# Performance work log

Measured on AMD Instinct MI355X. Metric: run time of the kernel, lower is better.

## Reference

```python
import jax, jax.numpy as jnp
import numpy as np

B, S, D = 8, 2048, 64
H = 128


def setup_inputs() -> dict:
    key = jax.random.key(0)
    k = jax.random.split(key, 5)
    X = jax.random.normal(k[0], (B, S, D), dtype=jnp.float32)
    Wi = jax.random.normal(k[1], (H, D), dtype=jnp.float32)          # init_layer weight, std=1
    bi = jax.random.normal(k[2], (H,), dtype=jnp.float32)            # init_layer bias, std=1
    Wa = jax.random.normal(k[3], (H * H, D + 1), dtype=jnp.float32) / jnp.sqrt(H)  # vf_A, std=1/sqrt(H)
    Wb = jax.random.normal(k[4], (H, D + 1), dtype=jnp.float32)      # vf_B, std=1
    return {"X": X, "Wi": Wi, "bi": bi, "Wa": Wa, "Wb": Wb}


def reference(X, Wi, bi, Wa, Wb):
    b, s, d = X.shape
    dt = 1.0 / (s - 1)
    # inp: time channel (constant dt) concatenated with scaled input -> [b, s, d+1]
    inp = jnp.concatenate([jnp.full((b, s, 1), dt, dtype=X.dtype), X * dt], axis=-1)
    y0 = X[:, 0] @ Wi.T + bi                       # [b, H]
    Bs = jnp.einsum('bsk,hk->bsh', inp[:, 1:], Wb)  # [b, s-1, H]

    def step(y, xs):
        inp_t, b_t = xs                            # [b, d+1], [b, H]
        A = (inp_t @ Wa.T).reshape(b, H, H)        # per-step transition matrix
        y_new = y + jnp.einsum('bij,bj->bi', A, y) + b_t
        return y_new, y_new

    xs = (jnp.swapaxes(inp[:, 1:], 0, 1), jnp.swapaxes(Bs, 0, 1))  # time-major
    _, ys_rest = jax.lax.scan(step, y0, xs)        # [s-1, b, H]
    ys = jnp.concatenate([y0[:, None, :], jnp.swapaxes(ys_rest, 0, 1)], axis=1)
    return ys
```

## Files before the change

### kernel.cpp

```cpp
#include <hip/hip_runtime.h>
#include <hip/hip_fp16.h>


typedef _Float16 h8 __attribute__((ext_vector_type(8)));
typedef float v4f __attribute__((ext_vector_type(4)));
typedef unsigned int uint;

constexpr int B_ = 8, S_ = 2048, D_ = 64, H_ = 128;
constexpr int T_ = S_ - 1;
constexpr int KD = D_ + 1;
constexpr float DTC = 1.0f / 2047.0f;
constexpr int L_ = 8;
constexpr int LSH = 3;
constexpr int NC = 256;

__global__ __launch_bounds__(256) void k_prep0(const float* __restrict__ Wa,
                                               _Float16* __restrict__ Wa16B,
                                               float* __restrict__ Wa0,
                                               const float* __restrict__ X,
                                               _Float16* __restrict__ Xs16) {
  int bx = blockIdx.x;
  if (bx < 4096) {
    int idx = bx * 256 + threadIdx.x;
    int r = idx >> 6, kk = idx & 63;
    int rt = r >> 4, n = r & 15;
    int kb = kk >> 5, q = (kk >> 3) & 3, jj = kk & 7;
    float v = Wa[(size_t)r * KD + 1 + kk];
    Wa16B[((((size_t)rt * 2 + kb) * 4 + q) * 16 + n) * 8 + jj] = (_Float16)v;
    if (kk == 0) Wa0[r] = Wa[(size_t)r * KD];
  } else {
    int idx = (bx - 4096) * 256 + threadIdx.x;
    if (idx < B_ * T_ * 64) {
      int bt = idx >> 6, d = idx & 63;
      int b = bt / T_, s = bt - b * T_;
      Xs16[(size_t)bt * 64 + d] = (_Float16)(X[((size_t)b * S_ + s + 1) * D_ + d] * DTC);
    }
  }
}

__global__ __launch_bounds__(256) void k_prep1(const float* __restrict__ X,
                                               const float* __restrict__ Wb,
                                               float* __restrict__ Bs,
                                               const float* __restrict__ Wi,
                                               const float* __restrict__ bi,
                                               float* __restrict__ out,
                                               float* __restrict__ yb) {
  int tid = threadIdx.x;
  if (blockIdx.x >= 1024) {
    int b = blockIdx.x - 1024;
    __shared__ float xs0[D_];
    if (tid < D_) xs0[tid] = X[(size_t)b * S_ * D_ + tid];
    __syncthreads();
    if (tid < H_) {
      float acc = bi[tid];
      const float* wr = Wi + tid * D_;
#pragma unroll 8
      for (int d = 0; d < D_; d++) acc += xs0[d] * wr[d];
      out[(size_t)b * S_ * H_ + tid] = acc;
      yb[(size_t)(b * NC + 0) * H_ + tid] = acc;
    }
    return;
  }
  __shared__ float wb_s[H_ * KD];
  __shared__ float xs[16][D_ + 4];
  int bt0 = blockIdx.x * 16;
  for (int i = tid; i < H_ * KD; i += 256) wb_s[i] = Wb[i];
  for (int i = tid; i < 16 * D_; i += 256) {
    int sl = i >> 6, d = i & 63;
    int btg = bt0 + sl;
    float v = 0.f;
    if (btg < B_ * T_) {
      int b = btg / T_, s = btg - b * T_;
      v = X[((size_t)b * S_ + s + 1) * D_ + d] * DTC;
    }
    xs[sl][d] = v;
  }
  __syncthreads();
  int h = tid & 127, sh = tid >> 7;
  const float* wrow = &wb_s[h * KD];
  for (int u = 0; u < 8; u++) {
    int sl = sh * 8 + u;
    int btg = bt0 + sl;
    if (btg >= B_ * T_) break;
    float acc = wrow[0] * DTC;
#pragma unroll 8
    for (int d = 0; d < D_; d++) acc += xs[sl][d] * wrow[1 + d];
    Bs[(size_t)btg * H_ + h] = acc;
  }
}

__global__ __launch_bounds__(256) void k_amat(const _Float16* __restrict__ Xs16,
                                              const _Float16* __restrict__ Wa16B,
                                              const float* __restrict__ Wa0,
                                              _Float16* __restrict__ A_sl,
                                              int c0, int scShift) {
  __shared__ _Float16 sb[32 * 528];
  int tid = threadIdx.x;
  int w = tid >> 6, lane = tid & 63;
  int n = lane & 15, q = lane >> 4;
  int rowbase = blockIdx.x * 32;
  int SCm = ((1 << scShift) << LSH) - 1;

  h8 af[2][2];
#pragma unroll
  for (int mi = 0; mi < 2; mi++) {
    int sidx = rowbase + mi * 16 + n;
    int b = sidx >> (scShift + LSH);
    int rem = sidx & SCm;
    int cc = rem >> LSH, l = rem & (L_ - 1);
    int s = (c0 + cc) * L_ + l;
    if (s >= T_) s = T_ - 1;
    size_t btg = (size_t)b * T_ + s;
#pragma unroll
    for (int kb = 0; kb < 2; kb++)
      af[mi][kb] = *(const h8*)(Xs16 + btg * 64 + kb * 32 + q * 8);
  }

  v4f acc[2][8];
#pragma unroll
  for (int nj = 0; nj < 8; nj++) {
    int ct_g = blockIdx.y * 32 + w * 8 + nj;
    float binit = DTC * Wa0[ct_g * 16 + n];
    h8 bf0 = *(const h8*)(Wa16B + ((((size_t)ct_g * 2 + 0) * 4 + q) * 16 + n) * 8);
    h8 bf1 = *(const h8*)(Wa16B + ((((size_t)ct_g * 2 + 1) * 4 + q) * 16 + n) * 8);
#pragma unroll
    for (int mi = 0; mi < 2; mi++) {
      v4f a;
      a[0] = binit; a[1] = binit; a[2] = binit; a[3] = binit;
      a = __builtin_amdgcn_mfma_f32_16x16x32_f16(af[mi][0], bf0, a, 0, 0, 0);
      a = __builtin_amdgcn_mfma_f32_16x16x32_f16(af[mi][1], bf1, a, 0, 0, 0);
      acc[mi][nj] = a;
    }
  }
#pragma unroll
  for (int mi = 0; mi < 2; mi++)
#pragma unroll
    for (int nj = 0; nj < 8; nj++)
#pragma unroll
      for (int reg = 0; reg < 4; reg++)
        sb[(mi * 16 + q * 4 + reg) * 528 + w * 128 + ((nj * 16 + n) ^ (q * 16))] =
            (_Float16)acc[mi][nj][reg];
  __syncthreads();
#pragma unroll
  for (int it = 0; it < 8; it++) {
    int idx = tid + it * 256;
    int t = idx >> 6, u4 = idx & 63;
    int qt = (t >> 2) & 3;
    uint4 val = *(const uint4*)&sb[t * 528 + ((u4 * 8) ^ (qt * 16))];
    *(uint4*)(A_sl + (size_t)(rowbase + t) * 16384 + blockIdx.y * 512 + u4 * 8) = val;
  }
}

__global__ __launch_bounds__(256) void k_chunkmap(const _Float16* __restrict__ A_sl,
                                                  const float* __restrict__ Bs,
                                                  _Float16* __restrict__ Mr,
                                                  float* __restrict__ vch,
                                                  int c0, int scShift) {
  __shared__ _Float16 Dt[128 * 136];
  __shared__ float v32[128];
  int tid = threadIdx.x;
  int w = tid >> 6, lane = tid & 63;
  int n = lane & 15, q = lane >> 4;
  int chunk = blockIdx.x;
  int SC = 1 << scShift;
  int b = chunk >> scShift;
  int cc = chunk & (SC - 1);
  int c = c0 + cc;
  int sbase = c * L_;
  int nsteps = min(L_, T_ - sbase);
  const _Float16* Abase = A_sl + (size_t)chunk * L_ * 16384;
  size_t btb = (size_t)b * T_ + sbase;

#pragma unroll
  for (int it = 0; it < 8; it++) {
    int idx = tid + it * 256;
    int rowl = idx & 127, c8 = (idx >> 7) * 8;
    uint4 pk = *(const uint4*)(Abase + rowl * 128 + c8);
    const _Float16* hp = (const _Float16*)&pk;
#pragma unroll
    for (int cx = 0; cx < 8; cx++) Dt[(c8 + cx) * 136 + rowl] = hp[cx];
  }
  if (tid < 128) v32[tid] = Bs[btb * 128 + tid];
  h8 idE, idO;
#pragma unroll
  for (int jj = 0; jj < 8; jj++) {
    idE[jj] = (_Float16)((q * 8 + jj == n) ? 1.f : 0.f);
    idO[jj] = (_Float16)((q * 8 + jj == 16 + n) ? 1.f : 0.f);
  }
  __syncthreads();

  v4f acc[2][8];
#pragma unroll
  for (int mi = 0; mi < 2; mi++) {
    int row0 = (2 * w + mi) * 16 + q * 4;
#pragma unroll
    for (int nj = 0; nj < 8; nj++) {
      int col = nj * 16 + n;
      union { uint2 u; _Float16 h[4]; } m2;
      m2.u = *(const uint2*)&Dt[col * 136 + row0];
#pragma unroll
      for (int reg = 0; reg < 4; reg++) acc[mi][nj][reg] = (float)m2.h[reg];
    }
  }

  int r0 = 2 * w * 16 + n, r1 = r0 + 16;
  h8 afA[2][4], afB[2][4];

#define LOADA(dst, l)                                                                \
  {                                                                                  \
    const _Float16* Ag = Abase + (size_t)(l) * 16384;                                \
    _Pragma("unroll")                                                                \
    for (int mi = 0; mi < 2; mi++)                                                   \
      _Pragma("unroll")                                                              \
      for (int kb = 0; kb < 4; kb++)                                                 \
        dst[mi][kb] = *(const h8*)(Ag + ((2 * w + mi) * 16 + n) * 128 + kb * 32 + q * 8); \
  }

#define STEPQ(af, l)                                                                 \
  {                                                                                  \
    _Pragma("unroll")                                                                \
    for (int nj = 0; nj < 8; nj++) {                                                 \
      h8 bfr[4];                                                                     \
      _Pragma("unroll")                                                              \
      for (int kb = 0; kb < 4; kb++)                                                 \
        bfr[kb] = *(const h8*)&Dt[(nj * 16 + n) * 136 + kb * 32 + q * 8];            \
      _Pragma("unroll")                                                              \
      for (int mi = 0; mi < 2; mi++) {                                               \
        _Pragma("unroll")                                                            \
        for (int kb = 0; kb < 4; kb++)                                               \
          acc[mi][nj] = __builtin_amdgcn_mfma_f32_16x16x32_f16(af[mi][kb], bfr[kb], acc[mi][nj], 0, 0, 0); \
        acc[mi][nj] = __builtin_amdgcn_mfma_f32_16x16x32_f16(                        \
            af[mi][nj >> 1], (nj & 1) ? idO : idE, acc[mi][nj], 0, 0, 0);            \
      }                                                                              \
    }                                                                                \
    float dv0 = 0.f, dv1 = 0.f;                                                      \
    _Pragma("unroll")                                                                \
    for (int kb = 0; kb < 4; kb++) {                                                 \
      float4 p0 = *(const float4*)&v32[kb * 32 + q * 8];                             \
      float4 p1 = *(const float4*)&v32[kb * 32 + q * 8 + 4];                         \
      float vk[8] = {p0.x, p0.y, p0.z, p0.w, p1.x, p1.y, p1.z, p1.w};                \
      _Pragma("unroll")                                                              \
      for (int jj = 0; jj < 8; jj++) {                                               \
        dv0 += (float)af[0][kb][jj] * vk[jj];                                        \
        dv1 += (float)af[1][kb][jj] * vk[jj];                                        \
      }                                                                              \
    }                                                                                \
    dv0 += __shfl_xor(dv0, 16); dv0 += __shfl_xor(dv0, 32);                          \
    dv1 += __shfl_xor(dv1, 16); dv1 += __shfl_xor(dv1, 32);                          \
    float vold0 = v32[r0], vold1 = v32[r1];                                          \
    float bs0 = 0.f, bs1 = 0.f;                                                      \
    if (q == 0) {                                                                    \
      bs0 = Bs[(btb + (l)) * 128 + r0];                                              \
      bs1 = Bs[(btb + (l)) * 128 + r1];                                              \
    }                                                                                \
    __syncthreads();                                                                 \
    _Pragma("unroll")                                                                \
    for (int mi = 0; mi < 2; mi++) {                                                 \
      int row0 = (2 * w + mi) * 16 + q * 4;                                          \
      _Pragma("unroll")                                                              \
      for (int nj = 0; nj < 8; nj++) {                                               \
        int col = nj * 16 + n;                                                       \
        union { _Float16 h[4]; uint2 u; } pk;                                        \
        _Pragma("unroll")                                                            \
        for (int reg = 0; reg < 4; reg++) pk.h[reg] = (_Float16)acc[mi][nj][reg];    \
        *(uint2*)&Dt[col * 136 + row0] = pk.u;                                       \
      }                                                                              \
    }                                                                                \
    if (q == 0) {                                                                    \
      v32[r0] = vold0 + dv0 + bs0;                                                   \
      v32[r1] = vold1 + dv1 + bs1;                                                   \
    }                                                                                \
    __syncthreads();                                                                 \
  }

  LOADA(afA, 1);
  for (int l = 1; l < nsteps; l += 2) {
    if (l + 1 < nsteps) LOADA(afB, l + 1);
    STEPQ(afA, l);
    if (l + 2 < nsteps) LOADA(afA, l + 2);
    if (l + 1 < nsteps) STEPQ(afB, l + 1);
  }
#undef LOADA
#undef STEPQ

#pragma unroll
  for (int mi = 0; mi < 2; mi++) {
    int row0 = (2 * w + mi) * 16 + q * 4;
#pragma unroll
    for (int nj = 0; nj < 8; nj++) {
      int col = nj * 16 + n;
#pragma unroll
      for (int reg = 0; reg < 4; reg++)
        Dt[(row0 + reg) * 136 + col] = (_Float16)acc[mi][nj][reg];
    }
  }
  __syncthreads();
  _Float16* og = Mr + (size_t)chunk * 16384;
#pragma unroll
  for (int it = 0; it < 8; it++) {
    int idx = tid + it * 256;
    int rowl = idx >> 4, ch = idx & 15;
    uint4 val = *(const uint4*)&Dt[rowl * 136 + ch * 8];
    *(uint4*)(og + rowl * 128 + ch * 8) = val;
  }
  if (tid < 128) vch[(size_t)chunk * 128 + tid] = v32[tid];
}

__global__ __launch_bounds__(256) void k_comp4(const _Float16* __restrict__ in_map,
                                               const float* __restrict__ in_v,
                                               _Float16* __restrict__ out_map,
                                               float* __restrict__ out_v) {
  __shared__ _Float16 Dt[128 * 136];
  __shared__ float v32[128];
  int tid = threadIdx.x;
  int w = tid >> 6, lane = tid & 63;
  int n = lane & 15, q = lane >> 4;
  size_t nbase = (size_t)blockIdx.x * 4;

  const _Float16* P0 = in_map + nbase * 16384;
#pragma unroll
  for (int it = 0; it < 8; it++) {
    int idx = tid + it * 256;
    int rowl = idx & 127, c8 = (idx >> 7) * 8;
    uint4 pk = *(const uint4*)(P0 + rowl * 128 + c8);
    const _Float16* hp = (const _Float16*)&pk;
#pragma unroll
    for (int cx = 0; cx < 8; cx++) Dt[(c8 + cx) * 136 + rowl] = hp[cx];
  }
  if (tid < 128) v32[tid] = in_v[nbase * 128 + tid];
  h8 idE, idO;
#pragma unroll
  for (int jj = 0; jj < 8; jj++) {
    idE[jj] = (_Float16)((q * 8 + jj == n) ? 1.f : 0.f);
    idO[jj] = (_Float16)((q * 8 + jj == 16 + n) ? 1.f : 0.f);
  }
  __syncthreads();

  v4f acc[2][8];
#pragma unroll
  for (int mi = 0; mi < 2; mi++) {
    int row0 = (2 * w + mi) * 16 + q * 4;
#pragma unroll
    for (int nj = 0; nj < 8; nj++) {
      int col = nj * 16 + n;
      union { uint2 u; _Float16 h[4]; } m2;
      m2.u = *(const uint2*)&Dt[col * 136 + row0];
#pragma unroll
      for (int reg = 0; reg < 4; reg++) acc[mi][nj][reg] = (float)m2.h[reg];
    }
  }

  int r0 = 2 * w * 16 + n, r1 = r0 + 16;
  for (int j = 1; j < 4; j++) {
    const _Float16* Pj = in_map + (nbase + j) * 16384;
    h8 af[2][4];
#pragma unroll
    for (int mi = 0; mi < 2; mi++)
#pragma unroll
      for (int kb = 0; kb < 4; kb++)
        af[mi][kb] = *(const h8*)(Pj + ((2 * w + mi) * 16 + n) * 128 + kb * 32 + q * 8);
#pragma unroll
    for (int nj = 0; nj < 8; nj++) {
      h8 bfr[4];
#pragma unroll
      for (int kb = 0; kb < 4; kb++)
        bfr[kb] = *(const h8*)&Dt[(nj * 16 + n) * 136 + kb * 32 + q * 8];
#pragma unroll
      for (int mi = 0; mi < 2; mi++) {
#pragma unroll
        for (int kb = 0; kb < 4; kb++)
          acc[mi][nj] = __builtin_amdgcn_mfma_f32_16x16x32_f16(af[mi][kb], bfr[kb], acc[mi][nj], 0, 0, 0);
        acc[mi][nj] = __builtin_amdgcn_mfma_f32_16x16x32_f16(
            af[mi][nj >> 1], (nj & 1) ? idO : idE, acc[mi][nj], 0, 0, 0);
      }
    }
    float dv0 = 0.f, dv1 = 0.f;
#pragma unroll
    for (int kb = 0; kb < 4; kb++) {
      float4 p0 = *(const float4*)&v32[kb * 32 + q * 8];
      float4 p1 = *(const float4*)&v32[kb * 32 + q * 8 + 4];
      float vk[8] = {p0.x, p0.y, p0.z, p0.w, p1.x, p1.y, p1.z, p1.w};
#pragma unroll
      for (int jj = 0; jj < 8; jj++) {
        dv0 += (float)af[0][kb][jj] * vk[jj];
        dv1 += (float)af[1][kb][jj] * vk[jj];
      }
    }
    dv0 += __shfl_xor(dv0, 16); dv0 += __shfl_xor(dv0, 32);
    dv1 += __shfl_xor(dv1, 16); dv1 += __shfl_xor(dv1, 32);
    float vold0 = v32[r0], vold1 = v32[r1];
    float vj0 = 0.f, vj1 = 0.f;
    if (q == 0) {
      vj0 = in_v[(nbase + j) * 128 + r0];
      vj1 = in_v[(nbase + j) * 128 + r1];
    }
    __syncthreads();
#pragma unroll
    for (int mi = 0; mi < 2; mi++) {
      int row0 = (2 * w + mi) * 16 + q * 4;
#pragma unroll
      for (int nj = 0; nj < 8; nj++) {
        int col = nj * 16 + n;
        union { _Float16 h[4]; uint2 u; } pk;
#pragma unroll
        for (int reg = 0; reg < 4; reg++) pk.h[reg] = (_Float16)acc[mi][nj][reg];
        *(uint2*)&Dt[col * 136 + row0] = pk.u;
      }
    }
    if (q == 0) {
      v32[r0] = vold0 + dv0 + vj0;
      v32[r1] = vold1 + dv1 + vj1;
    }
    __syncthreads();
  }
#pragma unroll
  for (int mi = 0; mi < 2; mi++) {
    int row0 = (2 * w + mi) * 16 + q * 4;
#pragma unroll
    for (int nj = 0; nj < 8; nj++) {
      int col = nj * 16 + n;
#pragma unroll
      for (int reg = 0; reg < 4; reg++)
        Dt[(row0 + reg) * 136 + col] = (_Float16)acc[mi][nj][reg];
    }
  }
  __syncthreads();
  _Float16* og = out_map + (size_t)blockIdx.x * 16384;
#pragma unroll
  for (int it = 0; it < 8; it++) {
    int idx = tid + it * 256;
    int rowl = idx >> 4, ch = idx & 15;
    uint4 val = *(const uint4*)&Dt[rowl * 136 + ch * 8];
    *(uint4*)(og + rowl * 128 + ch * 8) = val;
  }
  if (tid < 128) out_v[(size_t)blockIdx.x * 128 + tid] = v32[tid];
}

__global__ __launch_bounds__(256) void k_chainsuper(const _Float16* __restrict__ Sr,
                                                    const float* __restrict__ sv,
                                                    float* __restrict__ yb,
                                                    int c0, int scShift) {
  int b = blockIdx.x, tid = threadIdx.x;
  int NS = 1 << (scShift - 2);
  int i = tid >> 1, hh = tid & 1;
  __shared__ float ybuf[128];
  __shared__ float red[128];
  if (tid < 128) ybuf[tid] = yb[(size_t)(b * NC + c0) * 128 + tid];
  __syncthreads();

  uint4 arA[8], arB[8];
  float svA, svB;

#define LOADS(ar, svv, s)                                                            \
  {                                                                                  \
    const uint4* p = (const uint4*)(Sr + (size_t)(b * NS + (s)) * 16384 + i * 128 + hh * 64); \
    _Pragma("unroll")                                                                \
    for (int u = 0; u < 8; u++) ar[u] = p[u];                                        \
    svv = sv[(size_t)(b * NS + (s)) * 128 + i];                                      \
  }

#define STEPS(ar, svv, s)                                                            \
  {                                                                                  \
    float pt = 0.f;                                                                  \
    _Pragma("unroll")                                                                \
    for (int u = 0; u < 8; u++) {                                                    \
      union { uint4 v; _Float16 h[8]; } wv; wv.v = ar[u];                            \
      _Pragma("unroll")                                                              \
      for (int k = 0; k < 8; k++) pt += (float)wv.h[k] * ybuf[hh * 64 + u * 8 + k];  \
    }                                                                                \
    if (hh) red[i] = pt;                                                             \
    __syncthreads();                                                                 \
    if (!hh) {                                                                       \
      float yn = ybuf[i] + pt + red[i] + svv;                                        \
      int cg = c0 + 4 * ((s) + 1);                                                   \
      if (cg < NC) yb[(size_t)(b * NC + cg) * 128 + i] = yn;                         \
      ybuf[i] = yn;                                                                  \
    }                                                                                \
    __syncthreads();                                                                 \
  }

  LOADS(arA, svA, 0);
  int s = 0;
  for (; s + 1 < NS; s += 2) {
    LOADS(arB, svB, s + 1);
    STEPS(arA, svA, s);
    if (s + 2 < NS) LOADS(arA, svA, s + 2);
    STEPS(arB, svB, s + 1);
  }
  if (s < NS) STEPS(arA, svA, s);
#undef LOADS
#undef STEPS
}

__global__ __launch_bounds__(256) void k_emit(const _Float16* __restrict__ A_sl,
                                              const float* __restrict__ Bs,
                                              const _Float16* __restrict__ Mr,
                                              const float* __restrict__ vch,
                                              const float* __restrict__ yb,
                                              float* __restrict__ out,
                                              int c0, int scShift) {
  int tid = threadIdx.x;
  int SC = 1 << scShift;
  int b = blockIdx.x >> scShift;
  int cc = blockIdx.x & (SC - 1);
  int c = c0 + cc;
  int i = tid >> 1, hh = tid & 1;
  __shared__ float ybuf[128];
  __shared__ float red[128];
  int kpre = cc & 3;
  int cbase = c - kpre;
  if (tid < 128) ybuf[tid] = yb[(size_t)(b * NC + cbase) * 128 + tid];
  __syncthreads();
  size_t node0 = ((size_t)b << scShift) + (cc & ~3);

  uint4 arA[8], arB[8];
  float bsA, bsB;

  for (int j = 0; j < kpre; j++) {
    const uint4* p = (const uint4*)(Mr + (node0 + j) * 16384 + i * 128 + hh * 64);
#pragma unroll
    for (int u = 0; u < 8; u++) arA[u] = p[u];
    float vv = vch[(node0 + j) * 128 + i];
    float pt = 0.f;
#pragma unroll
    for (int u = 0; u < 8; u++) {
      union { uint4 v; _Float16 h[8]; } wv; wv.v = arA[u];
#pragma unroll
      for (int k = 0; k < 8; k++) pt += (float)wv.h[k] * ybuf[hh * 64 + u * 8 + k];
    }
    if (hh) red[i] = pt;
    __syncthreads();
    if (!hh) {
      float yn = ybuf[i] + pt + red[i] + vv;
      ybuf[i] = yn;
    }
    __syncthreads();
  }

  int nst = min(L_, T_ - c * L_);
  size_t sidx0 = (size_t)blockIdx.x * L_;
  size_t btb = (size_t)b * T_ + c * L_;

#define LOADR(ar, bsv, l)                                                            \
  {                                                                                  \
    const uint4* p = (const uint4*)(A_sl + (sidx0 + (l)) * 16384 + i * 128 + hh * 64); \
    _Pragma("unroll")                                                                \
    for (int u = 0; u < 8; u++) ar[u] = p[u];                                        \
    bsv = Bs[(btb + (l)) * 128 + i];                                                 \
  }

#define STEPE(ar, bsv, l)                                                            \
  {                                                                                  \
    float pt = 0.f;                                                                  \
    _Pragma("unroll")                                                                \
    for (int u = 0; u < 8; u++) {                                                    \
      union { uint4 v; _Float16 h[8]; } wv; wv.v = ar[u];                            \
      _Pragma("unroll")                                                              \
      for (int k = 0; k < 8; k++) pt += (float)wv.h[k] * ybuf[hh * 64 + u * 8 + k];  \
    }                                                                                \
    if (hh) red[i] = pt;                                                             \
    __syncthreads();                                                                 \
    if (!hh) {                                                                       \
      float yn = ybuf[i] + pt + red[i] + bsv;                                        \
      out[((size_t)b * S_ + (size_t)(c * L_ + (l) + 1)) * 128 + i] = yn;             \
      ybuf[i] = yn;                                                                  \
    }                                                                                \
    __syncthreads();                                                                 \
  }

  LOADR(arA, bsA, 0);
  for (int l = 0; l < nst; l += 2) {
    if (l + 1 < nst) LOADR(arB, bsB, l + 1);
    STEPE(arA, bsA, l);
    if (l + 2 < nst) LOADR(arA, bsA, l + 2);
    if (l + 1 < nst) STEPE(arB, bsB, l + 1);
  }
#undef LOADR
#undef STEPE
}

__global__ __launch_bounds__(256) void k_seq(const float* __restrict__ X,
                                             const float* __restrict__ Wa,
                                             const float* __restrict__ Wb,
                                             float* __restrict__ out) {
  int b = blockIdx.x, tid = threadIdx.x;
  int i = tid >> 1, hh = tid & 1;
  __shared__ float y[H_], red[H_], xs[D_], bts[H_];
  if (tid < H_) y[tid] = out[(size_t)b * S_ * H_ + tid];
  __syncthreads();
  for (int t = 1; t < S_; t++) {
    if (tid < D_) xs[tid] = X[((size_t)b * S_ + t) * D_ + tid] * DTC;
    __syncthreads();
    if (tid < H_) {
      const float* wr = Wb + tid * KD;
      float acc = wr[0] * DTC;
#pragma unroll 8
      for (int d = 0; d < D_; d++) acc += xs[d] * wr[1 + d];
      bts[tid] = acc;
    }
    float part = 0.f;
    const float* yhalf = &y[hh * 64];
    for (int j = 0; j < 64; j++) {
      const float* wr = Wa + ((size_t)(i * H_) + hh * 64 + j) * KD;
      float a = wr[0] * DTC;
#pragma unroll 8
      for (int d = 0; d < D_; d++) a += xs[d] * wr[1 + d];
      part += a * yhalf[j];
    }
    if (hh) red[i] = part;
    __syncthreads();
    if (!hh) {
      float yn = y[i] + part + red[i] + bts[i];
      out[((size_t)b * S_ + t) * H_ + i] = yn;
      y[i] = yn;
    }
    __syncthreads();
  }
}

__global__ __launch_bounds__(128) void k_y0f(const float* __restrict__ X,
                                             const float* __restrict__ Wi,
                                             const float* __restrict__ bi,
                                             float* __restrict__ out) {
  int b = blockIdx.x, h = threadIdx.x;
  __shared__ float xs[D_];
  if (h < D_) xs[h] = X[(size_t)b * S_ * D_ + h];
  __syncthreads();
  float acc = bi[h];
  const float* wr = Wi + h * D_;
#pragma unroll 8
  for (int d = 0; d < D_; d++) acc += xs[d] * wr[d];
  out[(size_t)b * S_ * H_ + h] = acc;
}

extern "C" void kernel_launch(void* const* d_in, const int* in_sizes, int n_in,
                              void* d_out, int out_size, void* d_ws, size_t ws_size,
                              hipStream_t stream) {
  (void)in_sizes; (void)n_in; (void)out_size;
  const float* X  = (const float*)d_in[0];
  const float* Wi = (const float*)d_in[1];
  const float* bi = (const float*)d_in[2];
  const float* Wa = (const float*)d_in[3];
  const float* Wb = (const float*)d_in[4];
  float* out = (float*)d_out;
  char* ws = (char*)d_ws;

  size_t off = 0;
  auto alloc = [&](size_t bytes) { size_t o = off; off = (off + bytes + 255) & ~(size_t)255; return o; };
  size_t oBs  = alloc((size_t)B_ * T_ * 128 * 4);
  size_t oYb  = alloc((size_t)B_ * NC * 128 * 4);
  size_t oWaB = alloc((size_t)64 * 16384 * 2);
  size_t oWa0 = alloc((size_t)16384 * 4);
  size_t oXs  = alloc((size_t)B_ * T_ * 64 * 2);
  size_t fixed = off;

  const size_t APC  = (size_t)B_ * L_ * 16384 * 2;
  const size_t MRPC = (size_t)B_ * 16384 * 2;
  const size_t VCPC = (size_t)B_ * 128 * 4;
  const size_t SRPC = (size_t)B_ * 16384 * 2 / 4;
  const size_t SVPC = (size_t)B_ * 128;
  const size_t PER_SC = APC + MRPC + VCPC + SRPC + SVPC + 5 * 256;

  int SC = 0;
  if (ws_size > fixed) {
    size_t avail = ws_size - fixed;
    SC = 64;
    while (SC >= 4 && (size_t)SC * PER_SC > avail) SC >>= 1;
    if (SC < 4) SC = 0;
  }
  if (SC < 4) {
    k_y0f<<<B_, 128, 0, stream>>>(X, Wi, bi, out);
    k_seq<<<B_, 256, 0, stream>>>(X, Wa, Wb, out);
    return;
  }
  int scShift = __builtin_ctz(SC);

  size_t oMr = alloc((size_t)SC * MRPC);
  size_t oVc = alloc((size_t)SC * VCPC);
  size_t oSr = alloc((size_t)SC * SRPC);
  size_t oSv = alloc((size_t)SC * SVPC);
  size_t oA  = alloc((size_t)SC * APC);

  float*    Bs    = (float*)(ws + oBs);
  float*    yb    = (float*)(ws + oYb);
  _Float16* Wa16B = (_Float16*)(ws + oWaB);
  float*    Wa0   = (float*)(ws + oWa0);
  _Float16* Xs16  = (_Float16*)(ws + oXs);
  _Float16* Mr    = (_Float16*)(ws + oMr);
  float*    vch   = (float*)(ws + oVc);
  _Float16* Sr    = (_Float16*)(ws + oSr);
  float*    sv    = (float*)(ws + oSv);
  _Float16* A_sl  = (_Float16*)(ws + oA);

  k_prep0<<<4096 + 4094, 256, 0, stream>>>(Wa, Wa16B, Wa0, X, Xs16);
  k_prep1<<<1024 + B_, 256, 0, stream>>>(X, Wb, Bs, Wi, bi, out, yb);

  int nslices = NC / SC;
  int chunks = B_ * SC;
  int amat_gx = (B_ * SC * L_) / 32;
  for (int si = 0; si < nslices; si++) {
    int c0 = si * SC;
    k_amat<<<dim3(amat_gx, 32), 256, 0, stream>>>(Xs16, Wa16B, Wa0, A_sl, c0, scShift);
    k_chunkmap<<<chunks, 256, 0, stream>>>(A_sl, Bs, Mr, vch, c0, scShift);
    k_comp4<<<chunks / 4, 256, 0, stream>>>(Mr, vch, Sr, sv);
    k_chainsuper<<<B_, 256, 0, stream>>>(Sr, sv, yb, c0, scShift);
    k_emit<<<chunks, 256, 0, stream>>>(A_sl, Bs, Mr, vch, yb, out, c0, scShift);
  }
}
```

Measured before the change: 608.3 us.

## Split chunk-map kernel columns across two blocks to double parallelism

Each chunk's 128-column transition map is now computed by two blocks, one per 64-column half. This halves the per-block accumulators and the LDS tile, and doubles the number of blocks launched. The goal is better occupancy and shorter per-block latency in the sequential chunk-map stage. In exchange, both blocks redundantly load the per-step A matrices. The vector (bias) recurrence is done only by the first column block, and the output transpose now uses an XOR-swizzled 72-wide LDS layout.

```diff
diff --git a/kernel.cpp b/kernel.cpp
--- a/kernel.cpp
+++ b/kernel.cpp
@@ -156,12 +156,14 @@
                                                   _Float16* __restrict__ Mr,
                                                   float* __restrict__ vch,
                                                   int c0, int scShift) {
-  __shared__ _Float16 Dt[128 * 136];
+  __shared__ _Float16 Dt[128 * 72];
   __shared__ float v32[128];
   int tid = threadIdx.x;
   int w = tid >> 6, lane = tid & 63;
   int n = lane & 15, q = lane >> 4;
-  int chunk = blockIdx.x;
+  int bx = blockIdx.x;
+  int chunk = ((bx >> 4) << 3) + (bx & 7);
+  int colblk = (bx >> 3) & 1;
   int SC = 1 << scShift;
   int b = chunk >> scShift;
   int cc = chunk & (SC - 1);
@@ -170,12 +172,13 @@
   int nsteps = min(L_, T_ - sbase);
   const _Float16* Abase = A_sl + (size_t)chunk * L_ * 16384;
   size_t btb = (size_t)b * T_ + sbase;
-
-#pragma unroll
-  for (int it = 0; it < 8; it++) {
+  int gc0 = colblk * 64;
+
+#pragma unroll
+  for (int it = 0; it < 4; it++) {
     int idx = tid + it * 256;
     int rowl = idx & 127, c8 = (idx >> 7) * 8;
-    uint4 pk = *(const uint4*)(Abase + rowl * 128 + c8);
+    uint4 pk = *(const uint4*)(Abase + rowl * 128 + gc0 + c8);
     const _Float16* hp = (const _Float16*)&pk;
 #pragma unroll
     for (int cx = 0; cx < 8; cx++) Dt[(c8 + cx) * 136 + rowl] = hp[cx];
@@ -189,15 +192,15 @@
   }
   __syncthreads();
 
-  v4f acc[2][8];
+  v4f acc[2][4];
 #pragma unroll
   for (int mi = 0; mi < 2; mi++) {
     int row0 = (2 * w + mi) * 16 + q * 4;
 #pragma unroll
-    for (int nj = 0; nj < 8; nj++) {
-      int col = nj * 16 + n;
+    for (int nj = 0; nj < 4; nj++) {
+      int lc = nj * 16 + n;
       union { uint2 u; _Float16 h[4]; } m2;
-      m2.u = *(const uint2*)&Dt[col * 136 + row0];
+      m2.u = *(const uint2*)&Dt[lc * 136 + row0];
 #pragma unroll
       for (int reg = 0; reg < 4; reg++) acc[mi][nj][reg] = (float)m2.h[reg];
     }
@@ -219,7 +222,8 @@
 #define STEPQ(af, l)                                                                 \
   {                                                                                  \
     _Pragma("unroll")                                                                \
-    for (int nj = 0; nj < 8; nj++) {                                                 \
+    for (int nj = 0; nj < 4; nj++) {                                                 \
+      int njg = colblk * 4 + nj;                                                     \
       h8 bfr[4];                                                                     \
       _Pragma("unroll")                                                              \
       for (int kb = 0; kb < 4; kb++)                                                 \
@@ -230,43 +234,43 @@
         for (int kb = 0; kb < 4; kb++)                                               \
           acc[mi][nj] = __builtin_amdgcn_mfma_f32_16x16x32_f16(af[mi][kb], bfr[kb], acc[mi][nj], 0, 0, 0); \
         acc[mi][nj] = __builtin_amdgcn_mfma_f32_16x16x32_f16(                        \
-            af[mi][nj >> 1], (nj & 1) ? idO : idE, acc[mi][nj], 0, 0, 0);            \
+            af[mi][njg >> 1], (njg & 1) ? idO : idE, acc[mi][nj], 0, 0, 0);          \
       }                                                                              \
     }                                                                                \
-    float dv0 = 0.f, dv1 = 0.f;                                                      \
-    _Pragma("unroll")                                                                \
-    for (int kb = 0; kb < 4; kb++) {                                                 \
-      float4 p0 = *(const float4*)&v32[kb * 32 + q * 8];                             \
-      float4 p1 = *(const float4*)&v32[kb * 32 + q * 8 + 4];                         \
-      float vk[8] = {p0.x, p0.y, p0.z, p0.w, p1.x, p1.y, p1.z, p1.w};                \
+    float dv0 = 0.f, dv1 = 0.f, vold0 = 0.f, vold1 = 0.f, bs0 = 0.f, bs1 = 0.f;      \
+    if (colblk == 0) {                                                               \
       _Pragma("unroll")                                                              \
-      for (int jj = 0; jj < 8; jj++) {                                               \
-        dv0 += (float)af[0][kb][jj] * vk[jj];                                        \
-        dv1 += (float)af[1][kb][jj] * vk[jj];                                        \
+      for (int kb = 0; kb < 4; kb++) {                                               \
+        float4 p0 = *(const float4*)&v32[kb * 32 + q * 8];                           \
+        float4 p1 = *(const float4*)&v32[kb * 32 + q * 8 + 4];                       \
+        float vk[8] = {p0.x, p0.y, p0.z, p0.w, p1.x, p1.y, p1.z, p1.w};              \
+        _Pragma("unroll")                                                            \
+        for (int jj = 0; jj < 8; jj++) {                                             \
+          dv0 += (float)af[0][kb][jj] * vk[jj];                                      \
+          dv1 += (float)af[1][kb][jj] * vk[jj];                                      \
+        }                                                                            \
       }                                                                              \
-    }                                                                                \
-    dv0 += __shfl_xor(dv0, 16); dv0 += __shfl_xor(dv0, 32);                          \
-    dv1 += __shfl_xor(dv1, 16); dv1 += __shfl_xor(dv1, 32);                          \
-    float vold0 = v32[r0], vold1 = v32[r1];                                          \
-    float bs0 = 0.f, bs1 = 0.f;                                                      \
-    if (q == 0) {                                                                    \
-      bs0 = Bs[(btb + (l)) * 128 + r0];                                              \
-      bs1 = Bs[(btb + (l)) * 128 + r1];                                              \
+      dv0 += __shfl_xor(dv0, 16); dv0 += __shfl_xor(dv0, 32);                        \
+      dv1 += __shfl_xor(dv1, 16); dv1 += __shfl_xor(dv1, 32);                        \
+      vold0 = v32[r0]; vold1 = v32[r1];                                              \
+      if (q == 0) {                                                                  \
+        bs0 = Bs[(btb + (l)) * 128 + r0];                                            \
+        bs1 = Bs[(btb + (l)) * 128 + r1];                                            \
+      }                                                                              \
     }                                                                                \
     __syncthreads();                                                                 \
     _Pragma("unroll")                                                                \
     for (int mi = 0; mi < 2; mi++) {                                                 \
       int row0 = (2 * w + mi) * 16 + q * 4;                                          \
       _Pragma("unroll")                                                              \
-      for (int nj = 0; nj < 8; nj++) {                                               \
-        int col = nj * 16 + n;                                                       \
+      for (int nj = 0; nj < 4; nj++) {                                               \
         union { _Float16 h[4]; uint2 u; } pk;                                        \
         _Pragma("unroll")                                                            \
         for (int reg = 0; reg < 4; reg++) pk.h[reg] = (_Float16)acc[mi][nj][reg];    \
-        *(uint2*)&Dt[col * 136 + row0] = pk.u;                                       \
+        *(uint2*)&Dt[(nj * 16 + n) * 136 + row0] = pk.u;                             \
       }                                                                              \
     }                                                                                \
-    if (q == 0) {                                                                    \
+    if (colblk == 0 && q == 0) {                                                     \
       v32[r0] = vold0 + dv0 + bs0;                                                   \
       v32[r1] = vold1 + dv1 + bs1;                                                   \
     }                                                                                \
@@ -287,23 +291,24 @@
   for (int mi = 0; mi < 2; mi++) {
     int row0 = (2 * w + mi) * 16 + q * 4;
 #pragma unroll
-    for (int nj = 0; nj < 8; nj++) {
-      int col = nj * 16 + n;
+    for (int nj = 0; nj < 4; nj++) {
+      int lcs = (nj * 16 + n) ^ (q * 16);
 #pragma unroll
       for (int reg = 0; reg < 4; reg++)
-        Dt[(row0 + reg) * 136 + col] = (_Float16)acc[mi][nj][reg];
+        Dt[(row0 + reg) * 72 + lcs] = (_Float16)acc[mi][nj][reg];
     }
   }
   __syncthreads();
   _Float16* og = Mr + (size_t)chunk * 16384;
 #pragma unroll
-  for (int it = 0; it < 8; it++) {
+  for (int it = 0; it < 4; it++) {
     int idx = tid + it * 256;
-    int rowl = idx >> 4, ch = idx & 15;
-    uint4 val = *(const uint4*)&Dt[rowl * 136 + ch * 8];
-    *(uint4*)(og + rowl * 128 + ch * 8) = val;
-  }
-  if (tid < 128) vch[(size_t)chunk * 128 + tid] = v32[tid];
+    int rowl = idx >> 3, ch = idx & 7;
+    int qr = (rowl >> 2) & 3;
+    uint4 val = *(const uint4*)&Dt[rowl * 72 + ((ch * 8) ^ (qr * 16))];
+    *(uint4*)(og + rowl * 128 + gc0 + ch * 8) = val;
+  }
+  if (colblk == 0 && tid < 128) vch[(size_t)chunk * 128 + tid] = v32[tid];
 }
 
 __global__ __launch_bounds__(256) void k_comp4(const _Float16* __restrict__ in_map,
@@ -701,7 +706,7 @@
   for (int si = 0; si < nslices; si++) {
     int c0 = si * SC;
     k_amat<<<dim3(amat_gx, 32), 256, 0, stream>>>(Xs16, Wa16B, Wa0, A_sl, c0, scShift);
-    k_chunkmap<<<chunks, 256, 0, stream>>>(A_sl, Bs, Mr, vch, c0, scShift);
+    k_chunkmap<<<2 * chunks, 256, 0, stream>>>(A_sl, Bs, Mr, vch, c0, scShift);
     k_comp4<<<chunks / 4, 256, 0, stream>>>(Mr, vch, Sr, sv);
     k_chainsuper<<<B_, 256, 0, stream>>>(Sr, sv, yb, c0, scShift);
     k_emit<<<chunks, 256, 0, stream>>>(A_sl, Bs, Mr, vch, yb, out, c0, scShift);
```

Result: slower. 2.196 ms (+260.9%).
